# Kernel optimization log

Hardware: AMD Instinct MI355X
Metric: run time of the kernel (lower is better)

Reference implementation:

```python
import jax, jax.numpy as jnp
import numpy as np

STAGE = 100
EPS = 1e-5


def bin_affine(w, shift_aff, sign_aff):
    """Vectorized equivalent of the 100-iteration range-mask loop.
    Original: for i in range(stage): mask = (w >= lo_i) & (w < hi_i);
              shift += w.detach()*shift_aff[i]*mask; sign += w.detach()*sign_aff[i]*mask.
    Equivalent to bucketize + gather + scale. Element equal to w.max() falls
    outside every half-open bin (strict <), so it gets zero, matching torch.
    w is detached in the original, so gradients flow only to the affines.
    """
    wf = w.reshape(-1)
    wmin, wmax = wf.min(), wf.max()
    t = (wf - wmin) / (wmax - wmin) * STAGE
    idx = jnp.floor(t).astype(jnp.int32)
    valid = (idx >= 0) & (idx < STAGE)
    idxc = jnp.clip(idx, 0, STAGE - 1)
    wd = jax.lax.stop_gradient(wf)
    shift = jnp.where(valid, wd * shift_aff[idxc], 0.0)
    sign = jnp.where(valid, wd * sign_aff[idxc], 0.0)
    return shift.reshape(w.shape), sign.reshape(w.shape)


def eff_weight(w, shift_aff, sign_aff):
    # Conv2dShift forward with externally-assigned continuous shift/sign:
    # effective weight = sign * 2**shift (deepshift-style, unrounded).
    shift, sign = bin_affine(w, shift_aff, sign_aff)
    return sign * jnp.exp2(shift)


def conv2d(x, w, stride=1, pad=0, groups=1):
    return jax.lax.conv_general_dilated(
        x, w, (stride, stride), [(pad, pad), (pad, pad)],
        dimension_numbers=("NCHW", "OIHW", "NCHW"), feature_group_count=groups)


def batchnorm(x, g, b):
    m = x.mean((0, 2, 3), keepdims=True)
    v = x.var((0, 2, 3), keepdims=True)
    return (x - m) * jax.lax.rsqrt(v + EPS) * g[None, :, None, None] + b[None, :, None, None]


def setup_inputs() -> dict:
    key = jax.random.key(0)
    ks = jax.random.split(key, 16)
    d = {
        "x": jax.random.normal(ks[0], (32, 256, 56, 56), jnp.float32),
        "w_ds": 0.05 * jax.random.normal(ks[1], (512, 256, 1, 1), jnp.float32),
        "w_c1": 0.05 * jax.random.normal(ks[2], (128, 256, 1, 1), jnp.float32),
        "w_peg": 0.05 * jax.random.normal(ks[3], (128, 1, 3, 3), jnp.float32),
        "w_c2": 0.05 * jax.random.normal(ks[4], (128, 128, 3, 3), jnp.float32),
        "w_c3": 0.05 * jax.random.normal(ks[5], (512, 128, 1, 1), jnp.float32),
        "aff_ds_shift": jax.random.normal(ks[6], (STAGE,), jnp.float32),
        "aff_ds_sign": jax.random.normal(ks[7], (STAGE,), jnp.float32),
        "aff_c1_shift": jax.random.normal(ks[8], (STAGE,), jnp.float32),
        "aff_c1_sign": jax.random.normal(ks[9], (STAGE,), jnp.float32),
        "aff_c2_shift": jax.random.normal(ks[10], (STAGE,), jnp.float32),
        "aff_c2_sign": jax.random.normal(ks[11], (STAGE,), jnp.float32),
        "aff_c3_shift": jax.random.normal(ks[12], (STAGE,), jnp.float32),
        "aff_c3_sign": jax.random.normal(ks[13], (STAGE,), jnp.float32),
        "g_bn_ds": jnp.ones((512,), jnp.float32),
        "b_bn_ds": jnp.zeros((512,), jnp.float32),
        "g_bn1": jnp.ones((128,), jnp.float32),
        "b_bn1": jnp.zeros((128,), jnp.float32),
        "g_bn2": jnp.ones((128,), jnp.float32),
        "b_bn2": jnp.zeros((128,), jnp.float32),
        "g_bn3": jnp.ones((512,), jnp.float32),
        "b_bn3": jnp.zeros((512,), jnp.float32),
    }
    return d


def reference(x, w_ds, w_c1, w_peg, w_c2, w_c3,
              aff_ds_shift, aff_ds_sign, aff_c1_shift, aff_c1_sign,
              aff_c2_shift, aff_c2_sign, aff_c3_shift, aff_c3_sign,
              g_bn_ds, b_bn_ds, g_bn1, b_bn1, g_bn2, b_bn2, g_bn3, b_bn3):
    # main branch (fmap_size == self.fmap_size): bin downsample + conv1/2/3 weights
    wds_e = eff_weight(w_ds, aff_ds_shift, aff_ds_sign)
    wc1_e = eff_weight(w_c1, aff_c1_shift, aff_c1_sign)
    wc2_e = eff_weight(w_c2, aff_c2_shift, aff_c2_sign)
    wc3_e = eff_weight(w_c3, aff_c3_shift, aff_c3_sign)

    # downsample = Conv1x1 -> BN -> ReLU
    residual = jax.nn.relu(batchnorm(conv2d(x, wds_e), g_bn_ds, b_bn_ds))

    h = conv2d(x, wc1_e)                                   # 1x1, 256->128
    h = conv2d(h, w_peg, stride=1, pad=1, groups=128)      # PEG depthwise 3x3
    h = jax.nn.relu(batchnorm(h, g_bn1, b_bn1))            # bn1 + act1
    h = conv2d(h, wc2_e, stride=1, pad=1)                  # 3x3, 128->128
    h = jax.nn.relu(batchnorm(h, g_bn2, b_bn2))            # bn2 + act2
    h = conv2d(h, wc3_e)                                   # 1x1, 128->512
    h = batchnorm(h, g_bn3, b_bn3)                         # bn3
    return jax.nn.relu(h + residual)                       # act3
```

## Files before the change

kernel.cpp:

```cpp
#include <hip/hip_runtime.h>
#include <stdint.h>


#define HW    3136
#define WID   56
#define NB    32
#define FLIP_TENSOR 1

#define OFF_MM    0
#define OFF_SC1   8
#define OFF_BI1   136
#define OFF_SC2   264
#define OFF_BI2   392
#define OFF_SC3   520
#define OFF_BI3   1032
#define OFF_SCDS  1544
#define OFF_BIDS  2056
#define WB_BASE_BYTES 16384ULL
#define WB_C1 0ULL
#define WB_C2 32768ULL
#define WB_C3 180224ULL
#define WB_DS 245760ULL
#define PS1S_B  786432ULL
#define PS1Q_B  802816ULL
#define PS2S_B  819200ULL
#define PS2Q_B  1622016ULL
#define PS3S_B  2424832ULL
#define PS3Q_B  5636096ULL
#define PSDS_B  8847360ULL
#define PSDQ_B  12058624ULL
#define AC_BASE_BYTES 16777216ULL
#define AC_A 0ULL
#define AC_B 12845056ULL
#define AC_C 25690112ULL
#define AC_R 77070336ULL
#define NSLOT 1568

typedef __attribute__((ext_vector_type(8))) short bfrag8;
typedef __attribute__((ext_vector_type(4))) float facc4;

__device__ __forceinline__ unsigned short f2bf(float f) {
  unsigned u = __float_as_uint(f);
  u = u + 0x7FFFu + ((u >> 16) & 1u);
  return (unsigned short)(u >> 16);
}
__device__ __forceinline__ float bf2f(unsigned short h) {
  return __uint_as_float(((unsigned)h) << 16);
}
__device__ __forceinline__ unsigned fmap(float f) {
  unsigned u = __float_as_uint(f);
  return (u & 0x80000000u) ? ~u : (u | 0x80000000u);
}
__device__ __forceinline__ float funmap(unsigned m) {
  unsigned u = (m & 0x80000000u) ? (m & 0x7FFFFFFFu) : ~m;
  return __uint_as_float(u);
}

__global__ void k_mm_init(unsigned* mm) {
  int t = threadIdx.x;
  if (t < 4) { mm[2 * t] = 0xFFFFFFFFu; mm[2 * t + 1] = 0u; }
}

__device__ __forceinline__ void tensor_of(int g0, int& tensor, int& local0) {
  if (g0 < 131072)      { tensor = 0; local0 = g0; }
  else if (g0 < 163840) { tensor = 1; local0 = g0 - 131072; }
  else if (g0 < 311296) { tensor = 2; local0 = g0 - 163840; }
  else                  { tensor = 3; local0 = g0 - 311296; }
}

__global__ __launch_bounds__(256) void k_minmax(
    const float* __restrict__ w_ds, const float* __restrict__ w_c1,
    const float* __restrict__ w_c2, const float* __restrict__ w_c3,
    unsigned* __restrict__ mm) {
  __shared__ unsigned smin[256], smax[256];
  int t = threadIdx.x;
  int tensor, local0;
  tensor_of(blockIdx.x * 1024, tensor, local0);
  const float* src = (tensor == 0) ? w_ds : (tensor == 1) ? w_c1 : (tensor == 2) ? w_c2 : w_c3;
  float4 v = *(const float4*)(src + local0 + t * 4);
  unsigned mn, mx;
  {
    unsigned m0 = fmap(v.x), m1 = fmap(v.y), m2 = fmap(v.z), m3 = fmap(v.w);
    mn = min(min(m0, m1), min(m2, m3));
    mx = max(max(m0, m1), max(m2, m3));
  }
  smin[t] = mn; smax[t] = mx;
  __syncthreads();
  for (int s = 128; s > 0; s >>= 1) {
    if (t < s) { smin[t] = min(smin[t], smin[t + s]); smax[t] = max(smax[t], smax[t + s]); }
    __syncthreads();
  }
  if (t == 0) {
    atomicMin(&mm[2 * tensor], smin[0]);
    atomicMax(&mm[2 * tensor + 1], smax[0]);
  }
}

__global__ __launch_bounds__(256) void k_effw(
    const float* __restrict__ w_ds, const float* __restrict__ w_c1,
    const float* __restrict__ w_c2, const float* __restrict__ w_c3,
    const float* __restrict__ sh_ds, const float* __restrict__ sg_ds,
    const float* __restrict__ sh_c1, const float* __restrict__ sg_c1,
    const float* __restrict__ sh_c2, const float* __restrict__ sg_c2,
    const float* __restrict__ sh_c3, const float* __restrict__ sg_c3,
    const unsigned* __restrict__ mm, unsigned short* __restrict__ wb) {
  int t = threadIdx.x;
  int tensor, local0;
  tensor_of(blockIdx.x * 1024, tensor, local0);
  const float* src = (tensor == 0) ? w_ds : (tensor == 1) ? w_c1 : (tensor == 2) ? w_c2 : w_c3;
  const float* sha = (tensor == 0) ? sh_ds : (tensor == 1) ? sh_c1 : (tensor == 2) ? sh_c2 : sh_c3;
  const float* sga = (tensor == 0) ? sg_ds : (tensor == 1) ? sg_c1 : (tensor == 2) ? sg_c2 : sg_c3;
  float wmin = funmap(mm[2 * tensor]);
  float wmax = funmap(mm[2 * tensor + 1]);
  float rng = __fsub_rn(wmax, wmin);
  float I32 = __fdiv_rn(rng, 100.0f);
  float edge100 = __fadd_rn(wmin, __fmul_rn(100.0f, I32));
  bool s32 = (wmax < edge100);
  bool binmax = (tensor == FLIP_TENSOR) ? !s32 : s32;
  float4 v4 = *(const float4*)(src + local0 + t * 4);
  float vs[4] = {v4.x, v4.y, v4.z, v4.w};
#pragma unroll
  for (int e = 0; e < 4; ++e) {
    int l = local0 + t * 4 + e;
    float v = vs[e];
    float ew;
    if (v == wmax) {
      ew = binmax ? (v * sga[99]) * exp2f(v * sha[99]) : 0.0f;
    } else {
      float tt = __fmul_rn(__fdiv_rn(__fsub_rn(v, wmin), rng), 100.0f);
      int idx = (int)floorf(tt);
      bool valid = (idx >= 0) && (idx < 100);
      int ic = valid ? idx : 0;
      float shift = valid ? v * sha[ic] : 0.0f;
      float sign  = valid ? v * sga[ic] : 0.0f;
      ew = sign * exp2f(shift);
    }
    unsigned short h = f2bf(ew);
    if (tensor == 0) {
      int co = l >> 8, ci = l & 255;
      wb[WB_DS + (size_t)co * 256 + ci] = h;
    } else if (tensor == 1) {
      int co = l >> 8, ci = l & 255;
      wb[WB_C1 + (size_t)co * 256 + ci] = h;
    } else if (tensor == 2) {
      int co = l / 1152; int r2 = l - co * 1152;
      int ci = r2 / 9; int tap = r2 - ci * 9;
      wb[WB_C2 + (size_t)co * 1152 + tap * 128 + ci] = h;
    } else {
      int co = l >> 7, ci = l & 127;
      wb[WB_C3 + (size_t)co * 128 + ci] = h;
    }
  }
}

template <int CI, int CO, int TAPS, int KBLK, bool XBF, bool YBF,
          bool FUSEIN, bool STATS, bool SWAP>
__global__ __launch_bounds__(256) void k_mconv4(
    const void* __restrict__ Xv, const unsigned short* __restrict__ Wt,
    void* __restrict__ Yv,
    const float* __restrict__ fsc, const float* __restrict__ fbi,
    float* __restrict__ PS, float* __restrict__ PQ) {
  constexpr int NSP = (TAPS == 9) ? 192 : 64;
  constexpr int ST  = KBLK + 2;
  __shared__ short lx[NSP][ST];
  __shared__ float redS[128][2], redQ[128][2];
  const int tid  = threadIdx.x;
  const int lane = tid & 63;
  const int wv   = tid >> 6;
  const int s0   = (SWAP ? blockIdx.y : blockIdx.x) * 64;
  const int co0  = (SWAP ? blockIdx.x : blockIdx.y) * 128;
  const int sx   = (SWAP ? blockIdx.y : blockIdx.x);
  const int n    = blockIdx.z;
  const int NK   = CI * TAPS;
  const unsigned short* Xh = (const unsigned short*)Xv + (size_t)n * CI * HW;
  const float*          Xf = (const float*)Xv + (size_t)n * CI * HW;

  const int wco  = (wv >> 1) * 64;
  const int wsp  = (wv & 1) * 32;
  const int lrow = lane & 15;
  const int lkg  = lane >> 4;
  const int kb8  = lkg * 8;

  int spl[2], yc[2], xc[2];
#pragma unroll
  for (int nn = 0; nn < 2; ++nn) {
    spl[nn] = wsp + nn * 16 + lrow;
    int s = s0 + spl[nn];
    yc[nn] = s / WID;
    xc[nn] = s - yc[nn] * WID;
  }

  facc4 acc[4][2];
#pragma unroll
  for (int m = 0; m < 4; ++m)
#pragma unroll
    for (int nn = 0; nn < 2; ++nn) acc[m][nn] = (facc4)(0.0f);

  for (int k0 = 0; k0 < CI; k0 += KBLK) {
    __syncthreads();
    if (TAPS == 9) {
#pragma unroll
      for (int i = 0; i < 3; ++i) {
        int task = tid + i * 256;
        int spi = task % 192;
        int kc  = task / 192;
        int p = s0 - 64 + spi;
        short v[8];
        if ((unsigned)p < (unsigned)HW) {
          const unsigned short* pp = Xh + (size_t)(k0 + kc * 8) * HW + p;
#pragma unroll
          for (int j = 0; j < 8; ++j) {
            if (FUSEIN) {
              float f = bf2f(pp[(size_t)j * HW]);
              f = fmaxf(fmaf(f, fsc[k0 + kc * 8 + j], fbi[k0 + kc * 8 + j]), 0.0f);
              v[j] = (short)f2bf(f);
            } else {
              v[j] = (short)pp[(size_t)j * HW];
            }
          }
        } else {
#pragma unroll
          for (int j = 0; j < 8; ++j) v[j] = 0;
        }
        *(short4*)(&lx[spi][kc * 8])     = (short4){v[0], v[1], v[2], v[3]};
        *(short4*)(&lx[spi][kc * 8 + 4]) = (short4){v[4], v[5], v[6], v[7]};
      }
    } else {
#pragma unroll
      for (int i = 0; i < KBLK / 32; ++i) {
        int task = tid + i * 256;
        int spi = task & 63;
        int kc  = task >> 6;
        int p = s0 + spi;
        short v[8];
        if (XBF) {
          const unsigned short* pp = Xh + (size_t)(k0 + kc * 8) * HW + p;
#pragma unroll
          for (int j = 0; j < 8; ++j) {
            if (FUSEIN) {
              float f = bf2f(pp[(size_t)j * HW]);
              f = fmaxf(fmaf(f, fsc[k0 + kc * 8 + j], fbi[k0 + kc * 8 + j]), 0.0f);
              v[j] = (short)f2bf(f);
            } else {
              v[j] = (short)pp[(size_t)j * HW];
            }
          }
        } else {
          const float* pf = Xf + (size_t)(k0 + kc * 8) * HW + p;
#pragma unroll
          for (int j = 0; j < 8; ++j) v[j] = (short)f2bf(pf[(size_t)j * HW]);
        }
        *(short4*)(&lx[spi][kc * 8])     = (short4){v[0], v[1], v[2], v[3]};
        *(short4*)(&lx[spi][kc * 8 + 4]) = (short4){v[4], v[5], v[6], v[7]};
      }
    }
    __syncthreads();
    if (TAPS == 1) {
      bfrag8 af[KBLK / 32][4];
#pragma unroll
      for (int kk = 0; kk < KBLK / 32; ++kk)
#pragma unroll
        for (int m = 0; m < 4; ++m)
          af[kk][m] = *(const bfrag8*)(Wt +
              (size_t)(co0 + wco + m * 16 + lrow) * NK + k0 + kk * 32 + kb8);
#pragma unroll
      for (int kk = 0; kk < KBLK / 32; ++kk) {
#pragma unroll
        for (int nn = 0; nn < 2; ++nn) {
          bfrag8 b = *(const bfrag8*)(&lx[spl[nn]][kk * 32 + kb8]);
#pragma unroll
          for (int m = 0; m < 4; ++m)
            acc[m][nn] = __builtin_amdgcn_mfma_f32_16x16x32_bf16(
                af[kk][m], b, acc[m][nn], 0, 0, 0);
        }
      }
    } else {
      bfrag8 afc[4], afn[4];
#pragma unroll
      for (int m = 0; m < 4; ++m)
        afc[m] = *(const bfrag8*)(Wt +
            (size_t)(co0 + wco + m * 16 + lrow) * NK + k0 + kb8);
      for (int tap = 0; tap < 9; ++tap) {
        if (tap < 8) {
#pragma unroll
          for (int m = 0; m < 4; ++m)
            afn[m] = *(const bfrag8*)(Wt +
                (size_t)(co0 + wco + m * 16 + lrow) * NK + (tap + 1) * CI + k0 + kb8);
        }
        const int dy = tap / 3 - 1;
        const int dx = tap % 3 - 1;
        const int off = dy * WID + dx;
#pragma unroll
        for (int nn = 0; nn < 2; ++nn) {
          bfrag8 b = *(const bfrag8*)(&lx[64 + spl[nn] + off][kb8]);
          bool valid = ((unsigned)(xc[nn] + dx) < (unsigned)WID) &&
                       ((unsigned)(yc[nn] + dy) < (unsigned)WID);
          if (!valid) b = (bfrag8)(short)0;
#pragma unroll
          for (int m = 0; m < 4; ++m)
            acc[m][nn] = __builtin_amdgcn_mfma_f32_16x16x32_bf16(
                afc[m], b, acc[m][nn], 0, 0, 0);
        }
#pragma unroll
        for (int m = 0; m < 4; ++m) afc[m] = afn[m];
      }
    }
  }
  unsigned short* Yh = (unsigned short*)Yv;
  float*          Yf = (float*)Yv;
#pragma unroll
  for (int m = 0; m < 4; ++m)
#pragma unroll
    for (int nn = 0; nn < 2; ++nn)
#pragma unroll
      for (int r = 0; r < 4; ++r) {
        int co_g = co0 + wco + m * 16 + lkg * 4 + r;
        int sp_g = s0 + wsp + nn * 16 + lrow;
        size_t addr = ((size_t)n * CO + co_g) * HW + sp_g;
        float v = acc[m][nn][r];
        if (YBF) Yh[addr] = f2bf(v); else Yf[addr] = v;
      }
  if (STATS) {
#pragma unroll
    for (int m = 0; m < 4; ++m)
#pragma unroll
      for (int r = 0; r < 4; ++r) {
        float sv = acc[m][0][r] + acc[m][1][r];
        float qv = acc[m][0][r] * acc[m][0][r] + acc[m][1][r] * acc[m][1][r];
#pragma unroll
        for (int d = 1; d < 16; d <<= 1) {
          sv += __shfl_xor(sv, d);
          qv += __shfl_xor(qv, d);
        }
        if (lrow == 0) {
          int col = wco + m * 16 + lkg * 4 + r;
          redS[col][wv & 1] = sv;
          redQ[col][wv & 1] = qv;
        }
      }
    __syncthreads();
    if (tid < 128) {
      int slot = n * 49 + sx;
      PS[(size_t)(co0 + tid) * NSLOT + slot] = redS[tid][0] + redS[tid][1];
      PQ[(size_t)(co0 + tid) * NSLOT + slot] = redQ[tid][0] + redQ[tid][1];
    }
  }
}

__global__ __launch_bounds__(256) void k_dw(
    const unsigned short* __restrict__ Xin, const float* __restrict__ wp,
    unsigned short* __restrict__ Yout,
    float* __restrict__ PS, float* __restrict__ PQ) {
  __shared__ float pl[HW];
  __shared__ float rs[256], rq[256];
  int bid = blockIdx.x;
  int c = bid & 127;
  int n = bid >> 7;
  const unsigned short* src = Xin + (size_t)bid * HW;
  int t = threadIdx.x;
  for (int q = t; q < HW / 4; q += 256) {
    ushort4 h4 = *(const ushort4*)(src + q * 4);
    pl[q * 4 + 0] = bf2f(h4.x); pl[q * 4 + 1] = bf2f(h4.y);
    pl[q * 4 + 2] = bf2f(h4.z); pl[q * 4 + 3] = bf2f(h4.w);
  }
  float w[9];
#pragma unroll
  for (int k = 0; k < 9; ++k) w[k] = wp[c * 9 + k];
  __syncthreads();
  unsigned short* dst = Yout + (size_t)bid * HW;
  float accS = 0.0f, accQ = 0.0f;
  for (int q = t; q < HW / 4; q += 256) {
    float o[4];
#pragma unroll
    for (int e = 0; e < 4; ++e) {
      int s = q * 4 + e;
      int y = s / WID, xcc = s - y * WID;
      float accv = 0.0f;
#pragma unroll
      for (int ky = 0; ky < 3; ++ky) {
        int yy = y + ky - 1;
        if (yy < 0 || yy >= WID) continue;
#pragma unroll
        for (int kx = 0; kx < 3; ++kx) {
          int xx = xcc + kx - 1;
          if (xx < 0 || xx >= WID) continue;
          accv = fmaf(w[ky * 3 + kx], pl[yy * WID + xx], accv);
        }
      }
      o[e] = accv;
      accS += accv;
      accQ = fmaf(accv, accv, accQ);
    }
    ushort4 ov;
    ov.x = f2bf(o[0]); ov.y = f2bf(o[1]); ov.z = f2bf(o[2]); ov.w = f2bf(o[3]);
    *(ushort4*)(dst + q * 4) = ov;
  }
  rs[t] = accS; rq[t] = accQ;
  __syncthreads();
  for (int st = 128; st > 0; st >>= 1) {
    if (t < st) { rs[t] += rs[t + st]; rq[t] += rq[t + st]; }
    __syncthreads();
  }
  if (t == 0) {
    PS[(size_t)c * NB + n] = rs[0];
    PQ[(size_t)c * NB + n] = rq[0];
  }
}

__global__ __launch_bounds__(256) void k_red(
    const float* __restrict__ S, const float* __restrict__ Q,
    const float* __restrict__ g, const float* __restrict__ b,
    float* __restrict__ sc_o, float* __restrict__ bi_o, int npart) {
  int c = blockIdx.x, t = threadIdx.x;
  double s = 0.0, q = 0.0;
  for (int i = t; i < npart; i += 256) {
    s += S[(size_t)c * npart + i];
    q += Q[(size_t)c * npart + i];
  }
  __shared__ double ss[256], qq[256];
  ss[t] = s; qq[t] = q;
  __syncthreads();
  for (int st = 128; st > 0; st >>= 1) {
    if (t < st) { ss[t] += ss[t + st]; qq[t] += qq[t + st]; }
    __syncthreads();
  }
  if (t == 0) {
    double nn = (double)HW * NB;
    double mean = ss[0] / nn;
    double var = qq[0] / nn - mean * mean;
    float rstd = (float)(1.0 / sqrt(var + 1e-5));
    float sc = g[c] * rstd;
    sc_o[c] = sc;
    bi_o[c] = b[c] - (float)mean * sc;
  }
}

__global__ __launch_bounds__(256) void k_final(
    float* __restrict__ out, const unsigned short* __restrict__ hC,
    const unsigned short* __restrict__ r,
    const float* __restrict__ sc3, const float* __restrict__ bi3,
    const float* __restrict__ scds, const float* __restrict__ bids) {
  const int QPN = 512 * 784;
  const int total = NB * QPN;
  for (int q = blockIdx.x * 256 + threadIdx.x; q < total; q += gridDim.x * 256) {
    int qn = q % QPN;
    int c = qn / 784;
    ushort4 hh = *(const ushort4*)(hC + (size_t)q * 4);
    ushort4 rh = *(const ushort4*)(r + (size_t)q * 4);
    float s3 = sc3[c], b3 = bi3[c], sd = scds[c], bd = bids[c];
    float4 o;
    float rb;
    rb = fmaxf(fmaf(bf2f(rh.x), sd, bd), 0.0f); o.x = fmaxf(fmaf(bf2f(hh.x), s3, b3) + rb, 0.0f);
    rb = fmaxf(fmaf(bf2f(rh.y), sd, bd), 0.0f); o.y = fmaxf(fmaf(bf2f(hh.y), s3, b3) + rb, 0.0f);
    rb = fmaxf(fmaf(bf2f(rh.z), sd, bd), 0.0f); o.z = fmaxf(fmaf(bf2f(hh.z), s3, b3) + rb, 0.0f);
    rb = fmaxf(fmaf(bf2f(rh.w), sd, bd), 0.0f); o.w = fmaxf(fmaf(bf2f(hh.w), s3, b3) + rb, 0.0f);
    *(float4*)(out + (size_t)q * 4) = o;
  }
}

extern "C" void kernel_launch(void* const* d_in, const int* in_sizes, int n_in,
                              void* d_out, int out_size, void* d_ws, size_t ws_size,
                              hipStream_t stream) {
  const float *x = nullptr, *w_ds = nullptr, *w_c1 = nullptr, *w_peg = nullptr,
              *w_c2 = nullptr, *w_c3 = nullptr;
  const float* aff[8] = {nullptr};
  const float* v512[4] = {nullptr};
  const float* v128[4] = {nullptr};
  int naff = 0, n512 = 0, n128 = 0;
  for (int i = 0; i < n_in; ++i) {
    const float* p = (const float*)d_in[i];
    switch (in_sizes[i]) {
      case 25690112: x = p; break;
      case 131072:   w_ds = p; break;
      case 32768:    w_c1 = p; break;
      case 1152:     w_peg = p; break;
      case 147456:   w_c2 = p; break;
      case 65536:    w_c3 = p; break;
      case 100:      if (naff < 8) aff[naff++] = p; break;
      case 512:      if (n512 < 4) v512[n512++] = p; break;
      case 128:      if (n128 < 4) v128[n128++] = p; break;
      default: break;
    }
  }
  const float *a_ds_sh = aff[0], *a_ds_sg = aff[1], *a_c1_sh = aff[2], *a_c1_sg = aff[3];
  const float *a_c2_sh = aff[4], *a_c2_sg = aff[5], *a_c3_sh = aff[6], *a_c3_sg = aff[7];
  const float *g_ds = v512[0], *b_ds = v512[1], *g3 = v512[2], *b3 = v512[3];
  const float *g1 = v128[0], *b1 = v128[1], *g2 = v128[2], *b2 = v128[3];

  float* ws  = (float*)d_ws;
  float* out = (float*)d_out;
  unsigned* mm = (unsigned*)(ws + OFF_MM);
  unsigned short* wb = (unsigned short*)((char*)d_ws + WB_BASE_BYTES);
  unsigned short* ac = (unsigned short*)((char*)d_ws + AC_BASE_BYTES);
  unsigned short* bufA = ac + AC_A;
  unsigned short* bufB = ac + AC_B;
  unsigned short* bufC = ac + AC_C;
  unsigned short* bufR = ac + AC_R;
  float* ps1S = (float*)((char*)d_ws + PS1S_B);
  float* ps1Q = (float*)((char*)d_ws + PS1Q_B);
  float* ps2S = (float*)((char*)d_ws + PS2S_B);
  float* ps2Q = (float*)((char*)d_ws + PS2Q_B);
  float* ps3S = (float*)((char*)d_ws + PS3S_B);
  float* ps3Q = (float*)((char*)d_ws + PS3Q_B);
  float* psdS = (float*)((char*)d_ws + PSDS_B);
  float* psdQ = (float*)((char*)d_ws + PSDQ_B);

  k_mm_init<<<dim3(1), dim3(64), 0, stream>>>(mm);
  k_minmax<<<dim3(368), dim3(256), 0, stream>>>(w_ds, w_c1, w_c2, w_c3, mm);
  k_effw<<<dim3(368), dim3(256), 0, stream>>>(
      w_ds, w_c1, w_c2, w_c3,
      a_ds_sh, a_ds_sg, a_c1_sh, a_c1_sg, a_c2_sh, a_c2_sg, a_c3_sh, a_c3_sg,
      mm, wb);

  k_mconv4<256, 128, 1, 128, false, true, false, false, false>
      <<<dim3(49, 1, 32), dim3(256), 0, stream>>>(
      x, wb + WB_C1, bufA, nullptr, nullptr, nullptr, nullptr);
  k_dw<<<dim3(NB * 128), dim3(256), 0, stream>>>(bufA, w_peg, bufB, ps1S, ps1Q);
  k_red<<<dim3(128), dim3(256), 0, stream>>>(ps1S, ps1Q, g1, b1,
                                             ws + OFF_SC1, ws + OFF_BI1, NB);
  k_mconv4<128, 128, 9, 32, true, true, true, true, false>
      <<<dim3(49, 1, 32), dim3(256), 0, stream>>>(
      bufB, wb + WB_C2, bufA, ws + OFF_SC1, ws + OFF_BI1, ps2S, ps2Q);
  k_red<<<dim3(128), dim3(256), 0, stream>>>(ps2S, ps2Q, g2, b2,
                                             ws + OFF_SC2, ws + OFF_BI2, NSLOT);
  k_mconv4<128, 512, 1, 128, true, true, true, true, true>
      <<<dim3(4, 49, 32), dim3(256), 0, stream>>>(
      bufA, wb + WB_C3, bufC, ws + OFF_SC2, ws + OFF_BI2, ps3S, ps3Q);
  k_red<<<dim3(512), dim3(256), 0, stream>>>(ps3S, ps3Q, g3, b3,
                                             ws + OFF_SC3, ws + OFF_BI3, NSLOT);
  k_mconv4<256, 512, 1, 128, false, true, false, true, true>
      <<<dim3(4, 49, 32), dim3(256), 0, stream>>>(
      x, wb + WB_DS, bufR, nullptr, nullptr, psdS, psdQ);
  k_red<<<dim3(512), dim3(256), 0, stream>>>(psdS, psdQ, g_ds, b_ds,
                                             ws + OFF_SCDS, ws + OFF_BIDS, NSLOT);
  k_final<<<dim3(4096), dim3(256), 0, stream>>>(out, bufC, bufR,
                                                ws + OFF_SC3, ws + OFF_BI3,
                                                ws + OFF_SCDS, ws + OFF_BIDS);
}
```

Measured before the change: 572.1 us.

## Merge conv1 and downsample 1x1 convs into one GEMM with XCD-aware block mapping

The conv1 (256->128) and downsample (256->512) 1x1 convolutions both read x, so their weights are concatenated into one 640-row matrix and computed by a single launch. Each block routes its output to either the conv1 buffer or the residual buffer, and only downsample blocks write BN statistics. Block indices are also remapped to a 1D grid that groups work by XCD (lid&7) so that blocks sharing the same input tile and batch land on the same XCD for better L2 reuse. This saves one full read of the fp32 x tensor and one kernel launch, but moves the downsample BN reduction earlier in the sequence.

Measured after the change: 545.4 us. -4.7%, faster.

```diff
diff --git a/kernel.cpp b/kernel.cpp
--- a/kernel.cpp
+++ b/kernel.cpp
@@ -17,10 +17,9 @@
 #define OFF_SCDS  1544
 #define OFF_BIDS  2056
 #define WB_BASE_BYTES 16384ULL
-#define WB_C1 0ULL
-#define WB_C2 32768ULL
-#define WB_C3 180224ULL
-#define WB_DS 245760ULL
+#define WB_M  0ULL
+#define WB_C2 163840ULL
+#define WB_C3 311296ULL
 #define PS1S_B  786432ULL
 #define PS1Q_B  802816ULL
 #define PS2S_B  819200ULL
@@ -138,10 +137,10 @@
     unsigned short h = f2bf(ew);
     if (tensor == 0) {
       int co = l >> 8, ci = l & 255;
-      wb[WB_DS + (size_t)co * 256 + ci] = h;
+      wb[WB_M + (size_t)(128 + co) * 256 + ci] = h;
     } else if (tensor == 1) {
       int co = l >> 8, ci = l & 255;
-      wb[WB_C1 + (size_t)co * 256 + ci] = h;
+      wb[WB_M + (size_t)co * 256 + ci] = h;
     } else if (tensor == 2) {
       int co = l / 1152; int r2 = l - co * 1152;
       int ci = r2 / 9; int tap = r2 - ci * 9;
@@ -153,11 +152,11 @@
   }
 }
 
-template <int CI, int CO, int TAPS, int KBLK, bool XBF, bool YBF,
-          bool FUSEIN, bool STATS, bool SWAP>
-__global__ __launch_bounds__(256) void k_mconv4(
+template <int CI, int TAPS, int KBLK, int COOUT, bool XBF,
+          bool FUSEIN, bool STATS, bool MERGED, int NCOB>
+__global__ __launch_bounds__(256) void k_mconv6(
     const void* __restrict__ Xv, const unsigned short* __restrict__ Wt,
-    void* __restrict__ Yv,
+    unsigned short* __restrict__ Y1, unsigned short* __restrict__ Y2,
     const float* __restrict__ fsc, const float* __restrict__ fbi,
     float* __restrict__ PS, float* __restrict__ PQ) {
   constexpr int NSP = (TAPS == 9) ? 192 : 64;
@@ -167,11 +166,16 @@
   const int tid  = threadIdx.x;
   const int lane = tid & 63;
   const int wv   = tid >> 6;
-  const int s0   = (SWAP ? blockIdx.y : blockIdx.x) * 64;
-  const int co0  = (SWAP ? blockIdx.x : blockIdx.y) * 128;
-  const int sx   = (SWAP ? blockIdx.y : blockIdx.x);
-  const int n    = blockIdx.z;
-  const int NK   = CI * TAPS;
+  int lid = blockIdx.x;
+  int xcd = lid & 7;
+  int j   = lid >> 3;
+  int co_blk = j % NCOB;
+  int t_  = xcd * 196 + j / NCOB;
+  int sp_blk = t_ % 49;
+  int n      = t_ / 49;
+  const int s0  = sp_blk * 64;
+  const int co0 = co_blk * 128;
+  const int NK  = CI * TAPS;
   const unsigned short* Xh = (const unsigned short*)Xv + (size_t)n * CI * HW;
   const float*          Xf = (const float*)Xv + (size_t)n * CI * HW;
 
@@ -209,18 +213,18 @@
         if ((unsigned)p < (unsigned)HW) {
           const unsigned short* pp = Xh + (size_t)(k0 + kc * 8) * HW + p;
 #pragma unroll
-          for (int j = 0; j < 8; ++j) {
+          for (int jj = 0; jj < 8; ++jj) {
             if (FUSEIN) {
-              float f = bf2f(pp[(size_t)j * HW]);
-              f = fmaxf(fmaf(f, fsc[k0 + kc * 8 + j], fbi[k0 + kc * 8 + j]), 0.0f);
-              v[j] = (short)f2bf(f);
+              float f = bf2f(pp[(size_t)jj * HW]);
+              f = fmaxf(fmaf(f, fsc[k0 + kc * 8 + jj], fbi[k0 + kc * 8 + jj]), 0.0f);
+              v[jj] = (short)f2bf(f);
             } else {
-              v[j] = (short)pp[(size_t)j * HW];
+              v[jj] = (short)pp[(size_t)jj * HW];
             }
           }
         } else {
 #pragma unroll
-          for (int j = 0; j < 8; ++j) v[j] = 0;
+          for (int jj = 0; jj < 8; ++jj) v[jj] = 0;
         }
         *(short4*)(&lx[spi][kc * 8])     = (short4){v[0], v[1], v[2], v[3]};
         *(short4*)(&lx[spi][kc * 8 + 4]) = (short4){v[4], v[5], v[6], v[7]};
@@ -236,19 +240,19 @@
         if (XBF) {
           const unsigned short* pp = Xh + (size_t)(k0 + kc * 8) * HW + p;
 #pragma unroll
-          for (int j = 0; j < 8; ++j) {
+          for (int jj = 0; jj < 8; ++jj) {
             if (FUSEIN) {
-              float f = bf2f(pp[(size_t)j * HW]);
-              f = fmaxf(fmaf(f, fsc[k0 + kc * 8 + j], fbi[k0 + kc * 8 + j]), 0.0f);
-              v[j] = (short)f2bf(f);
+              float f = bf2f(pp[(size_t)jj * HW]);
+              f = fmaxf(fmaf(f, fsc[k0 + kc * 8 + jj], fbi[k0 + kc * 8 + jj]), 0.0f);
+              v[jj] = (short)f2bf(f);
             } else {
-              v[j] = (short)pp[(size_t)j * HW];
+              v[jj] = (short)pp[(size_t)jj * HW];
             }
           }
         } else {
           const float* pf = Xf + (size_t)(k0 + kc * 8) * HW + p;
 #pragma unroll
-          for (int j = 0; j < 8; ++j) v[j] = (short)f2bf(pf[(size_t)j * HW]);
+          for (int jj = 0; jj < 8; ++jj) v[jj] = (short)f2bf(pf[(size_t)jj * HW]);
         }
         *(short4*)(&lx[spi][kc * 8])     = (short4){v[0], v[1], v[2], v[3]};
         *(short4*)(&lx[spi][kc * 8 + 4]) = (short4){v[4], v[5], v[6], v[7]};
@@ -306,21 +310,26 @@
       }
     }
   }
-  unsigned short* Yh = (unsigned short*)Yv;
-  float*          Yf = (float*)Yv;
+  unsigned short* Yb;
+  int coL, COst;
+  if (MERGED) {
+    if (co0 < 128) { Yb = Y1; coL = co0; COst = 128; }
+    else           { Yb = Y2; coL = co0 - 128; COst = 512; }
+  } else {
+    Yb = Y1; coL = co0; COst = COOUT;
+  }
 #pragma unroll
   for (int m = 0; m < 4; ++m)
 #pragma unroll
     for (int nn = 0; nn < 2; ++nn)
 #pragma unroll
       for (int r = 0; r < 4; ++r) {
-        int co_g = co0 + wco + m * 16 + lkg * 4 + r;
+        int co_g = coL + wco + m * 16 + lkg * 4 + r;
         int sp_g = s0 + wsp + nn * 16 + lrow;
-        size_t addr = ((size_t)n * CO + co_g) * HW + sp_g;
-        float v = acc[m][nn][r];
-        if (YBF) Yh[addr] = f2bf(v); else Yf[addr] = v;
-      }
-  if (STATS) {
+        Yb[((size_t)n * COst + co_g) * HW + sp_g] = f2bf(acc[m][nn][r]);
+      }
+  const bool do_st = STATS && (!MERGED || co0 >= 128);
+  if (do_st) {
 #pragma unroll
     for (int m = 0; m < 4; ++m)
 #pragma unroll
@@ -340,9 +349,10 @@
       }
     __syncthreads();
     if (tid < 128) {
-      int slot = n * 49 + sx;
-      PS[(size_t)(co0 + tid) * NSLOT + slot] = redS[tid][0] + redS[tid][1];
-      PQ[(size_t)(co0 + tid) * NSLOT + slot] = redQ[tid][0] + redQ[tid][1];
+      int cstat = (MERGED ? co0 - 128 : co0) + tid;
+      int slot = n * 49 + sp_blk;
+      PS[(size_t)cstat * NSLOT + slot] = redS[tid][0] + redS[tid][1];
+      PQ[(size_t)cstat * NSLOT + slot] = redQ[tid][0] + redQ[tid][1];
     }
   }
 }
@@ -512,27 +522,24 @@
       a_ds_sh, a_ds_sg, a_c1_sh, a_c1_sg, a_c2_sh, a_c2_sg, a_c3_sh, a_c3_sg,
       mm, wb);
 
-  k_mconv4<256, 128, 1, 128, false, true, false, false, false>
-      <<<dim3(49, 1, 32), dim3(256), 0, stream>>>(
-      x, wb + WB_C1, bufA, nullptr, nullptr, nullptr, nullptr);
+  k_mconv6<256, 1, 128, 0, false, false, true, true, 5>
+      <<<dim3(7840), dim3(256), 0, stream>>>(
+      x, wb + WB_M, bufA, bufR, nullptr, nullptr, psdS, psdQ);
+  k_red<<<dim3(512), dim3(256), 0, stream>>>(psdS, psdQ, g_ds, b_ds,
+                                             ws + OFF_SCDS, ws + OFF_BIDS, NSLOT);
   k_dw<<<dim3(NB * 128), dim3(256), 0, stream>>>(bufA, w_peg, bufB, ps1S, ps1Q);
   k_red<<<dim3(128), dim3(256), 0, stream>>>(ps1S, ps1Q, g1, b1,
                                              ws + OFF_SC1, ws + OFF_BI1, NB);
-  k_mconv4<128, 128, 9, 32, true, true, true, true, false>
-      <<<dim3(49, 1, 32), dim3(256), 0, stream>>>(
-      bufB, wb + WB_C2, bufA, ws + OFF_SC1, ws + OFF_BI1, ps2S, ps2Q);
+  k_mconv6<128, 9, 32, 128, true, true, true, false, 1>
+      <<<dim3(1568), dim3(256), 0, stream>>>(
+      bufB, wb + WB_C2, bufA, nullptr, ws + OFF_SC1, ws + OFF_BI1, ps2S, ps2Q);
   k_red<<<dim3(128), dim3(256), 0, stream>>>(ps2S, ps2Q, g2, b2,
                                              ws + OFF_SC2, ws + OFF_BI2, NSLOT);
-  k_mconv4<128, 512, 1, 128, true, true, true, true, true>
-      <<<dim3(4, 49, 32), dim3(256), 0, stream>>>(
-      bufA, wb + WB_C3, bufC, ws + OFF_SC2, ws + OFF_BI2, ps3S, ps3Q);
+  k_mconv6<128, 1, 128, 512, true, true, true, false, 4>
+      <<<dim3(6272), dim3(256), 0, stream>>>(
+      bufA, wb + WB_C3, bufC, nullptr, ws + OFF_SC2, ws + OFF_BI2, ps3S, ps3Q);
   k_red<<<dim3(512), dim3(256), 0, stream>>>(ps3S, ps3Q, g3, b3,
                                              ws + OFF_SC3, ws + OFF_BI3, NSLOT);
-  k_mconv4<256, 512, 1, 128, false, true, false, true, true>
-      <<<dim3(4, 49, 32), dim3(256), 0, stream>>>(
-      x, wb + WB_DS, bufR, nullptr, nullptr, psdS, psdQ);
-  k_red<<<dim3(512), dim3(256), 0, stream>>>(psdS, psdQ, g_ds, b_ds,
-                                             ws + OFF_SCDS, ws + OFF_BIDS, NSLOT);
   k_final<<<dim3(4096), dim3(256), 0, stream>>>(out, bufC, bufR,
                                                 ws + OFF_SC3, ws + OFF_BI3,
                                                 ws + OFF_SCDS, ws + OFF_BIDS);
```
